# Kernel tuning notes

Measured on AMD Instinct MI355X. Metric: run time of the kernel, lower is better.

Reference implementation:

```python
import jax, jax.numpy as jnp
import numpy as np
import math

D_KEY = 64
D_VALUE = 64
NUM_HEADS = 16
D_MODEL = D_VALUE * NUM_HEADS  # 1024


def setup_inputs() -> dict:
    key = jax.random.key(0)
    ks = jax.random.split(key, 5)
    B, N = 2, 2048
    s = 1.0 / math.sqrt(D_MODEL)
    return {
        "x": jax.random.normal(ks[0], (B, N, D_MODEL), dtype=jnp.float32),
        "Wq": jax.random.normal(ks[1], (D_MODEL, D_KEY * NUM_HEADS), dtype=jnp.float32) * s,
        "Wk": jax.random.normal(ks[2], (D_MODEL, D_KEY * NUM_HEADS), dtype=jnp.float32) * s,
        "Wv": jax.random.normal(ks[3], (D_MODEL, D_MODEL), dtype=jnp.float32) * s,
        "Wp": jax.random.normal(ks[4], (D_MODEL, D_MODEL), dtype=jnp.float32) * s,
    }


def reference(x, Wq, Wk, Wv, Wp):
    # x: [B, N, d_model]. Equivalent to the original block-diagonal concat trick:
    # off-diagonal blocks are -inf, so softmax over the key axis reduces to
    # independent per-head softmax attention.
    B, N, D = x.shape
    H, K, V = NUM_HEADS, D_KEY, D_VALUE
    scale = 1.0 / math.sqrt(K)
    q = (x @ Wq).reshape(B, N, H, K)
    k = (x @ Wk).reshape(B, N, H, K)
    v = (x @ Wv).reshape(B, N, H, V)
    scores = jnp.einsum("bnhk,bmhk->bhnm", q, k) * scale  # [B,H,N,N]
    attn = jax.nn.softmax(scores, axis=-1)
    out = jnp.einsum("bhnm,bmhv->bnhv", attn, v).reshape(B, N, D)
    return x + out @ Wp
```

## Files before the change

### kernel.cpp

```cpp
#include <hip/hip_runtime.h>

typedef float f32x4 __attribute__((ext_vector_type(4)));
typedef __bf16 bf16x8 __attribute__((ext_vector_type(8)));

#define DEV static __device__ __forceinline__

DEV ushort f2bf(float f) {
  unsigned u = __builtin_bit_cast(unsigned, f);
  u += 0x7FFFu + ((u >> 16) & 1u);
  return (ushort)(u >> 16);
}

DEV bf16x8 ld_frag(const ushort* p) {
  return __builtin_bit_cast(bf16x8, *reinterpret_cast<const int4*>(p));
}

DEV bf16x8 ld_lds(const ushort* base, int byte_off) {
  return __builtin_bit_cast(bf16x8,
      *reinterpret_cast<const int4*>(reinterpret_cast<const char*>(base) + byte_off));
}

DEV int swz(int row, int col_byte) { return row * 128 + (col_byte ^ ((row & 7) << 4)); }

DEV float fast_exp2(float x) {
  float r;
  asm("v_exp_f32 %0, %1" : "=v"(r) : "v"(x));
  return r;
}

DEV unsigned cvt_pk_bf16(float lo, float hi) {
  unsigned r;
  asm("v_cvt_pk_bf16_f32 %0, %1, %2" : "=v"(r) : "v"(lo), "v"(hi));
  return r;
}

DEV void gload16(const ushort* g, ushort* l) {
  __builtin_amdgcn_global_load_lds(
      (const __attribute__((address_space(1))) unsigned int*)g,
      (__attribute__((address_space(3))) unsigned int*)l, 16, 0, 0);
}


__global__ __launch_bounds__(256) void prep(const float* __restrict__ x,
                                            const float* __restrict__ w0,
                                            const float* __restrict__ w1,
                                            const float* __restrict__ w2,
                                            const float* __restrict__ w3,
                                            ushort* __restrict__ xb,
                                            ushort* __restrict__ wt) {
  __shared__ float tile[32][33];
  const int z = blockIdx.z;
  const int tx = threadIdx.x, ty = threadIdx.y;
  if (z < 4) {
    const float* w = z == 0 ? w0 : z == 1 ? w1 : z == 2 ? w2 : w3;
    ushort* out = wt + (size_t)z * 1024 * 1024;
    const int n0 = blockIdx.x * 32, k0 = blockIdx.y * 32;
    float4 v = *reinterpret_cast<const float4*>(&w[(size_t)(k0 + ty) * 1024 + n0 + tx * 4]);
    tile[ty][tx * 4 + 0] = v.x;
    tile[ty][tx * 4 + 1] = v.y;
    tile[ty][tx * 4 + 2] = v.z;
    tile[ty][tx * 4 + 3] = v.w;
    __syncthreads();
    ushort4 o = make_ushort4(f2bf(tile[tx * 4 + 0][ty]), f2bf(tile[tx * 4 + 1][ty]),
                             f2bf(tile[tx * 4 + 2][ty]), f2bf(tile[tx * 4 + 3][ty]));
    *reinterpret_cast<ushort4*>(&out[(size_t)(n0 + ty) * 1024 + k0 + tx * 4]) = o;
  } else {
    const int blk = ((z - 4) * 32 + blockIdx.y) * 32 + blockIdx.x;
    const int tid = ty * 8 + tx;
    const int i = blk * 256 + tid;
    float4 v = reinterpret_cast<const float4*>(x)[i];
    ushort4 o = make_ushort4(f2bf(v.x), f2bf(v.y), f2bf(v.z), f2bf(v.w));
    reinterpret_cast<ushort4*>(xb)[i] = o;
  }
}


DEV void gemm_core64(const ushort* __restrict__ A, const ushort* __restrict__ BT,
                     ushort* a_lds, ushort* b_lds, int row0, int col0, f32x4 acc[4][2]) {
  const int tid = threadIdx.x;
  const int lane = tid & 63;
  const int w = tid >> 6, wr = w >> 1, wc = w & 1;
  const int lg = lane >> 4, l15 = lane & 15;
  const int sr8 = lane >> 3;
  const int scol = ((lane & 7) ^ sr8) << 3;
  const ushort* ga = A + (size_t)(row0 + w * 32 + sr8) * 1024 + scol;
  const ushort* gb = BT + (size_t)(col0 + w * 16 + sr8) * 1024 + scol;
#pragma unroll
  for (int ai = 0; ai < 4; ++ai)
#pragma unroll
    for (int bj = 0; bj < 2; ++bj) acc[ai][bj] = f32x4{0.f, 0.f, 0.f, 0.f};

  for (int kt = 0; kt < 1024; kt += 64) {
    __syncthreads();
#pragma unroll
    for (int p = 0; p < 4; ++p)
      gload16(ga + kt + (size_t)(p * 8) * 1024, a_lds + (w * 32 + p * 8) * 64);
#pragma unroll
    for (int p = 0; p < 2; ++p)
      gload16(gb + kt + (size_t)(p * 8) * 1024, b_lds + (w * 16 + p * 8) * 64);
    __syncthreads();
    bf16x8 af[4][2], bfr[2][2];
#pragma unroll
    for (int kk = 0; kk < 2; ++kk) {
#pragma unroll
      for (int i = 0; i < 4; ++i)
        af[i][kk] = ld_lds(a_lds, swz(wr * 64 + i * 16 + l15, kk * 64 + lg * 16));
#pragma unroll
      for (int j = 0; j < 2; ++j)
        bfr[j][kk] = ld_lds(b_lds, swz(wc * 32 + j * 16 + l15, kk * 64 + lg * 16));
    }
#pragma unroll
    for (int kk = 0; kk < 2; ++kk)
#pragma unroll
      for (int ai = 0; ai < 4; ++ai)
#pragma unroll
        for (int bj = 0; bj < 2; ++bj)
          acc[ai][bj] = __builtin_amdgcn_mfma_f32_16x16x32_bf16(af[ai][kk], bfr[bj][kk],
                                                                acc[ai][bj], 0, 0, 0);
  }
}

__global__ __launch_bounds__(256) void gemm_qkv(const ushort* __restrict__ xb,
                                                const ushort* __restrict__ wqT,
                                                const ushort* __restrict__ wkT,
                                                const ushort* __restrict__ wvT,
                                                ushort* __restrict__ q, ushort* __restrict__ k,
                                                ushort* __restrict__ vt) {
  __shared__ ushort a_lds[128 * 64], b_lds[64 * 64];
  const int fid = blockIdx.x;
  const int wid = (fid & 7) * 192 + (fid >> 3);
  const int row = wid / 48, rem = wid % 48;
  const int z = rem % 3, col = rem / 3;
  const int row0 = row * 128, col0 = col * 64;
  const ushort* BT = z == 0 ? wqT : z == 1 ? wkT : wvT;
  f32x4 acc[4][2];
  gemm_core64(xb, BT, a_lds, b_lds, row0, col0, acc);
  const int lane = threadIdx.x & 63;
  const int w = threadIdx.x >> 6, wr = w >> 1, wc = w & 1;
  const int lg = lane >> 4, l15 = lane & 15;
  if (z < 2) {
    ushort* out = z == 0 ? q : k;
    const float sc = z == 0 ? 0.125f * 1.4426950408889634f : 1.0f;
#pragma unroll
    for (int ai = 0; ai < 4; ++ai)
#pragma unroll
      for (int bj = 0; bj < 2; ++bj)
#pragma unroll
        for (int r = 0; r < 4; ++r) {
          int orow = row0 + wr * 64 + ai * 16 + lg * 4 + r;
          int ocol = col0 + wc * 32 + bj * 16 + l15;
          out[(size_t)orow * 1024 + ocol] = f2bf(acc[ai][bj][r] * sc);
        }
  } else {
#pragma unroll
    for (int ai = 0; ai < 4; ++ai)
#pragma unroll
      for (int bj = 0; bj < 2; ++bj) {
        int orow = row0 + wr * 64 + ai * 16 + lg * 4;
        int ocol = col0 + wc * 32 + bj * 16 + l15;
        int bb = orow >> 11, n = orow & 2047;
        ushort4 pk = make_ushort4(f2bf(acc[ai][bj][0]), f2bf(acc[ai][bj][1]),
                                  f2bf(acc[ai][bj][2]), f2bf(acc[ai][bj][3]));
        *reinterpret_cast<ushort4*>(vt + ((size_t)(bb * 1024 + ocol)) * 2048 + n) = pk;
      }
  }
}

__global__ __launch_bounds__(256) void gemm_out(const ushort* __restrict__ ob,
                                                const ushort* __restrict__ wpT,
                                                const float* __restrict__ x,
                                                float* __restrict__ y) {
  __shared__ ushort a_lds[64 * 64], b_lds[64 * 64];
  const int fid = blockIdx.x;
  const int wid = (fid & 7) * 128 + (fid >> 3);
  const int row0 = (wid >> 4) * 64, col0 = (wid & 15) * 64;
  const int tid = threadIdx.x;
  const int lane = tid & 63;
  const int w = tid >> 6, wr = w >> 1, wc = w & 1;
  const int lg = lane >> 4, l15 = lane & 15;
  const int sr8 = lane >> 3;
  const int scol = ((lane & 7) ^ sr8) << 3;
  const ushort* ga = ob + (size_t)(row0 + w * 16 + sr8) * 1024 + scol;
  const ushort* gb = wpT + (size_t)(col0 + w * 16 + sr8) * 1024 + scol;

  f32x4 acc[2][2];
#pragma unroll
  for (int ai = 0; ai < 2; ++ai)
#pragma unroll
    for (int bj = 0; bj < 2; ++bj) acc[ai][bj] = f32x4{0.f, 0.f, 0.f, 0.f};

  for (int kt = 0; kt < 1024; kt += 64) {
    __syncthreads();
#pragma unroll
    for (int p = 0; p < 2; ++p) {
      gload16(ga + kt + (size_t)(p * 8) * 1024, a_lds + (w * 16 + p * 8) * 64);
      gload16(gb + kt + (size_t)(p * 8) * 1024, b_lds + (w * 16 + p * 8) * 64);
    }
    __syncthreads();
    bf16x8 af[2][2], bfr[2][2];
#pragma unroll
    for (int kk = 0; kk < 2; ++kk) {
#pragma unroll
      for (int i = 0; i < 2; ++i) {
        af[i][kk] = ld_lds(a_lds, swz(wr * 32 + i * 16 + l15, kk * 64 + lg * 16));
        bfr[i][kk] = ld_lds(b_lds, swz(wc * 32 + i * 16 + l15, kk * 64 + lg * 16));
      }
    }
#pragma unroll
    for (int kk = 0; kk < 2; ++kk)
#pragma unroll
      for (int ai = 0; ai < 2; ++ai)
#pragma unroll
        for (int bj = 0; bj < 2; ++bj)
          acc[ai][bj] = __builtin_amdgcn_mfma_f32_16x16x32_bf16(af[ai][kk], bfr[bj][kk],
                                                                acc[ai][bj], 0, 0, 0);
  }

#pragma unroll
  for (int ai = 0; ai < 2; ++ai)
#pragma unroll
    for (int bj = 0; bj < 2; ++bj)
#pragma unroll
      for (int r = 0; r < 4; ++r) {
        int orow = row0 + wr * 32 + ai * 16 + lg * 4 + r;
        int ocol = col0 + wc * 32 + bj * 16 + l15;
        size_t idx = (size_t)orow * 1024 + ocol;
        y[idx] = x[idx] + acc[ai][bj][r];
      }
}

__global__ __launch_bounds__(256) void attn(const ushort* __restrict__ qg,
                                            const ushort* __restrict__ kg,
                                            const ushort* __restrict__ vtg,
                                            ushort* __restrict__ og) {
  __shared__ ushort k_lds[4 * 64 * 64];
  __shared__ ushort v_lds[4 * 64 * 64];
  const int fid = blockIdx.x;
  const int wid = (fid & 7) * 64 + (fid >> 3);
  const int bh = wid >> 4, q0 = wid & 15;
  const int b = bh >> 4, h = bh & 15;
  const int n0 = q0 * 128;
  const int tid = threadIdx.x, lane = tid & 63, w = tid >> 6;
  const int lg = lane >> 4, l15 = lane & 15;

  bf16x8 qf[2][2];
#pragma unroll
  for (int qi = 0; qi < 2; ++qi)
#pragma unroll
    for (int d32 = 0; d32 < 2; ++d32)
      qf[qi][d32] = ld_frag(qg + (size_t)(b * 2048 + n0 + w * 32 + qi * 16 + l15) * 1024 +
                            h * 64 + d32 * 32 + lg * 8);

  f32x4 o[2][4];
#pragma unroll
  for (int qi = 0; qi < 2; ++qi)
#pragma unroll
    for (int bj = 0; bj < 4; ++bj) o[qi][bj] = f32x4{0.f, 0.f, 0.f, 0.f};
  f32x4 ssum[2] = {f32x4{0.f, 0.f, 0.f, 0.f}, f32x4{0.f, 0.f, 0.f, 0.f}};

  const int sr8 = lane >> 3;
  const int scol = ((lane & 7) ^ sr8) << 3;
  const ushort* kbase = kg + (size_t)(b * 2048 + w * 16 + sr8) * 1024 + h * 64 + scol;
  const ushort* vbase = vtg + (size_t)(b * 1024 + h * 64 + w * 16 + sr8) * 2048 + scol;

  auto stage_sub = [&](ushort* kdst, ushort* vdst, int kv0) {
#pragma unroll
    for (int p = 0; p < 2; ++p) {
      gload16(kbase + (size_t)(kv0 + p * 8) * 1024, kdst + (w * 16 + p * 8) * 64);
      gload16(vbase + (size_t)(p * 8) * 2048 + kv0, vdst + (w * 16 + p * 8) * 64);
    }
  };
  auto stage2 = [&](int buf, int kv0) {
    stage_sub(k_lds + (2 * buf) * 4096, v_lds + (2 * buf) * 4096, kv0);
    stage_sub(k_lds + (2 * buf + 1) * 4096, v_lds + (2 * buf + 1) * 4096, kv0 + 64);
  };

  const int4 ones4 = make_int4(0x3F803F80, 0x3F803F80, 0x3F803F80, 0x3F803F80);
  const bf16x8 onesf = __builtin_bit_cast(bf16x8, ones4);

  auto qk_sub = [&](const ushort* kb, f32x4 s[2][4]) {
#pragma unroll
    for (int qi = 0; qi < 2; ++qi)
#pragma unroll
      for (int kj = 0; kj < 4; ++kj) s[qi][kj] = f32x4{0.f, 0.f, 0.f, 0.f};
#pragma unroll
    for (int d32 = 0; d32 < 2; ++d32)
#pragma unroll
      for (int kj = 0; kj < 4; ++kj) {
        bf16x8 kf = ld_lds(kb, swz(kj * 16 + l15, d32 * 64 + lg * 16));
        s[0][kj] = __builtin_amdgcn_mfma_f32_16x16x32_bf16(kf, qf[0][d32], s[0][kj], 0, 0, 0);
        s[1][kj] = __builtin_amdgcn_mfma_f32_16x16x32_bf16(kf, qf[1][d32], s[1][kj], 0, 0, 0);
      }
  };

  auto exp_pack = [&](f32x4 s[2][4], bf16x8 pa[2][2]) {
#pragma unroll
    for (int qi = 0; qi < 2; ++qi) {
      unsigned pk[4][2];
#pragma unroll
      for (int kj = 0; kj < 4; ++kj) {
        float p0 = fast_exp2(s[qi][kj][0]);
        float p1 = fast_exp2(s[qi][kj][1]);
        float p2 = fast_exp2(s[qi][kj][2]);
        float p3 = fast_exp2(s[qi][kj][3]);
        pk[kj][0] = cvt_pk_bf16(p0, p1);
        pk[kj][1] = cvt_pk_bf16(p2, p3);
      }
#pragma unroll
      for (int k32 = 0; k32 < 2; ++k32) {
        unsigned x0 = pk[2 * k32][0], y0 = pk[2 * k32 + 1][0];
        unsigned x1 = pk[2 * k32][1], y1 = pk[2 * k32 + 1][1];
        asm("v_permlane32_swap_b32 %0, %1" : "+v"(x0), "+v"(y0));
        asm("v_permlane32_swap_b32 %0, %1" : "+v"(x1), "+v"(y1));
        asm("v_permlane16_swap_b32 %0, %1" : "+v"(x0), "+v"(y0));
        asm("v_permlane16_swap_b32 %0, %1" : "+v"(x1), "+v"(y1));
        int4 fr = make_int4(x0, x1, y0, y1);
        pa[qi][k32] = __builtin_bit_cast(bf16x8, fr);
      }
    }
  };

  auto pv_only = [&](const ushort* vb, bf16x8 pa[2][2]) {
#pragma unroll
    for (int qi = 0; qi < 2; ++qi) {
      ssum[qi] = __builtin_amdgcn_mfma_f32_16x16x32_bf16(pa[qi][0], onesf, ssum[qi], 0, 0, 0);
      ssum[qi] = __builtin_amdgcn_mfma_f32_16x16x32_bf16(pa[qi][1], onesf, ssum[qi], 0, 0, 0);
    }
#pragma unroll
    for (int k32 = 0; k32 < 2; ++k32)
#pragma unroll
      for (int bj = 0; bj < 4; ++bj) {
        bf16x8 vf = ld_lds(vb, swz(bj * 16 + l15, k32 * 64 + lg * 16));
        o[0][bj] = __builtin_amdgcn_mfma_f32_16x16x32_bf16(pa[0][k32], vf, o[0][bj], 0, 0, 0);
        o[1][bj] = __builtin_amdgcn_mfma_f32_16x16x32_bf16(pa[1][k32], vf, o[1][bj], 0, 0, 0);
      }
  };

  auto body2 = [&](int buf) {
    const ushort* kb0 = k_lds + (2 * buf) * 4096;
    const ushort* kb1 = k_lds + (2 * buf + 1) * 4096;
    const ushort* vb0 = v_lds + (2 * buf) * 4096;
    const ushort* vb1 = v_lds + (2 * buf + 1) * 4096;
    f32x4 s0[2][4], s1[2][4];
    bf16x8 pa0[2][2], pa1[2][2];
    qk_sub(kb0, s0);
    qk_sub(kb1, s1);
    exp_pack(s0, pa0);
    pv_only(vb0, pa0);
    exp_pack(s1, pa1);
    pv_only(vb1, pa1);
    __builtin_amdgcn_sched_group_barrier(0x020, 8, 0);
    __builtin_amdgcn_sched_group_barrier(0x100, 8, 0);
    __builtin_amdgcn_sched_group_barrier(0x008, 16, 0);
    __builtin_amdgcn_sched_group_barrier(0x100, 8, 0);
#pragma unroll
    for (int i = 0; i < 16; ++i) {
      __builtin_amdgcn_sched_group_barrier(0x008, 1, 0);
      __builtin_amdgcn_sched_group_barrier(0x002, 4, 0);
    }
    __builtin_amdgcn_sched_group_barrier(0x100, 8, 0);
#pragma unroll
    for (int i = 0; i < 20; ++i) {
      __builtin_amdgcn_sched_group_barrier(0x008, 1, 0);
      __builtin_amdgcn_sched_group_barrier(0x002, 3, 0);
    }
    __builtin_amdgcn_sched_group_barrier(0x100, 8, 0);
    __builtin_amdgcn_sched_group_barrier(0x008, 20, 0);
  };

  stage2(0, 0);
  __syncthreads();

  for (int tt = 0; tt < 8; ++tt) {
    stage2(1, (2 * tt + 1) * 128);
    body2(0);
    __syncthreads();
    if (tt < 7) stage2(0, (2 * tt + 2) * 128);
    body2(1);
    __syncthreads();
  }

#pragma unroll
  for (int qi = 0; qi < 2; ++qi) {
    f32x4 inv;
#pragma unroll
    for (int r = 0; r < 4; ++r) inv[r] = 1.0f / ssum[qi][r];
#pragma unroll
    for (int bj = 0; bj < 4; ++bj)
#pragma unroll
      for (int r = 0; r < 4; ++r) {
        int n = n0 + w * 32 + qi * 16 + lg * 4 + r;
        og[(size_t)(b * 2048 + n) * 1024 + h * 64 + bj * 16 + l15] = f2bf(o[qi][bj][r] * inv[r]);
      }
  }
}


extern "C" void kernel_launch(void* const* d_in, const int* in_sizes, int n_in,
                              void* d_out, int out_size, void* d_ws, size_t ws_size,
                              hipStream_t stream) {
  const float* x = (const float*)d_in[0];
  const float* Wq = (const float*)d_in[1];
  const float* Wk = (const float*)d_in[2];
  const float* Wv = (const float*)d_in[3];
  const float* Wp = (const float*)d_in[4];
  float* y = (float*)d_out;

  char* ws = (char*)d_ws;
  ushort* xb = (ushort*)(ws);
  ushort* wT = (ushort*)(ws + (8ull << 20));
  ushort* qw = (ushort*)(ws + (16ull << 20));
  ushort* kw = (ushort*)(ws + (24ull << 20));
  ushort* vtw = (ushort*)(ws + (32ull << 20));
  ushort* ow = (ushort*)(ws);

  prep<<<dim3(32, 32, 8), dim3(8, 32), 0, stream>>>(x, Wq, Wk, Wv, Wp, xb, wT);
  gemm_qkv<<<1536, 256, 0, stream>>>(xb, wT, wT + (1u << 20), wT + (2u << 20), qw, kw, vtw);
  attn<<<512, 256, 0, stream>>>(qw, kw, vtw, ow);
  gemm_out<<<1024, 256, 0, stream>>>(ow, wT + (3u << 20), x, y);
}
```

Measured before the change: 105.6 us.

## Fuse Q/K/V projections into one block sharing the x tile

Each QKV GEMM block now computes the Q, K and V output tiles for the same row/column range in one pass, loading the x (A) tile into LDS once and reusing it across all three weight matrices. The grid shrinks from 1536 to 512 blocks and the block swizzle is adjusted. This removes two-thirds of the redundant A-tile loads, but triples the accumulator registers and increases LDS use, which may lower occupancy and leave fewer blocks to spread across the CUs.

```diff
diff --git a/kernel.cpp b/kernel.cpp
--- a/kernel.cpp
+++ b/kernel.cpp
@@ -74,21 +74,34 @@
   }
 }
 
-
-DEV void gemm_core64(const ushort* __restrict__ A, const ushort* __restrict__ BT,
-                     ushort* a_lds, ushort* b_lds, int row0, int col0, f32x4 acc[4][2]) {
+__global__ __launch_bounds__(256) void gemm_qkv(const ushort* __restrict__ xb,
+                                                const ushort* __restrict__ wT,
+                                                ushort* __restrict__ q, ushort* __restrict__ k,
+                                                ushort* __restrict__ vt) {
+  __shared__ ushort a_lds[128 * 64];
+  __shared__ ushort b_lds[3][64 * 64];
+  const int fid = blockIdx.x;
+  const int wid = (fid & 7) * 64 + (fid >> 3);
+  const int row0 = (wid >> 4) * 128, col0 = (wid & 15) * 64;
   const int tid = threadIdx.x;
   const int lane = tid & 63;
   const int w = tid >> 6, wr = w >> 1, wc = w & 1;
   const int lg = lane >> 4, l15 = lane & 15;
   const int sr8 = lane >> 3;
   const int scol = ((lane & 7) ^ sr8) << 3;
-  const ushort* ga = A + (size_t)(row0 + w * 32 + sr8) * 1024 + scol;
-  const ushort* gb = BT + (size_t)(col0 + w * 16 + sr8) * 1024 + scol;
-#pragma unroll
-  for (int ai = 0; ai < 4; ++ai)
-#pragma unroll
-    for (int bj = 0; bj < 2; ++bj) acc[ai][bj] = f32x4{0.f, 0.f, 0.f, 0.f};
+  const ushort* ga = xb + (size_t)(row0 + w * 32 + sr8) * 1024 + scol;
+  const ushort* gb[3];
+#pragma unroll
+  for (int z = 0; z < 3; ++z)
+    gb[z] = wT + (size_t)z * 1024 * 1024 + (size_t)(col0 + w * 16 + sr8) * 1024 + scol;
+
+  f32x4 acc[3][4][2];
+#pragma unroll
+  for (int z = 0; z < 3; ++z)
+#pragma unroll
+    for (int ai = 0; ai < 4; ++ai)
+#pragma unroll
+      for (int bj = 0; bj < 2; ++bj) acc[z][ai][bj] = f32x4{0.f, 0.f, 0.f, 0.f};
 
   for (int kt = 0; kt < 1024; kt += 64) {
     __syncthreads();
@@ -96,49 +109,38 @@
     for (int p = 0; p < 4; ++p)
       gload16(ga + kt + (size_t)(p * 8) * 1024, a_lds + (w * 32 + p * 8) * 64);
 #pragma unroll
-    for (int p = 0; p < 2; ++p)
-      gload16(gb + kt + (size_t)(p * 8) * 1024, b_lds + (w * 16 + p * 8) * 64);
-    __syncthreads();
-    bf16x8 af[4][2], bfr[2][2];
-#pragma unroll
-    for (int kk = 0; kk < 2; ++kk) {
+    for (int z = 0; z < 3; ++z)
+#pragma unroll
+      for (int p = 0; p < 2; ++p)
+        gload16(gb[z] + kt + (size_t)(p * 8) * 1024, b_lds[z] + (w * 16 + p * 8) * 64);
+    __syncthreads();
+    bf16x8 af[4][2];
+#pragma unroll
+    for (int kk = 0; kk < 2; ++kk)
 #pragma unroll
       for (int i = 0; i < 4; ++i)
         af[i][kk] = ld_lds(a_lds, swz(wr * 64 + i * 16 + l15, kk * 64 + lg * 16));
 #pragma unroll
-      for (int j = 0; j < 2; ++j)
-        bfr[j][kk] = ld_lds(b_lds, swz(wc * 32 + j * 16 + l15, kk * 64 + lg * 16));
-    }
-#pragma unroll
-    for (int kk = 0; kk < 2; ++kk)
-#pragma unroll
-      for (int ai = 0; ai < 4; ++ai)
-#pragma unroll
-        for (int bj = 0; bj < 2; ++bj)
-          acc[ai][bj] = __builtin_amdgcn_mfma_f32_16x16x32_bf16(af[ai][kk], bfr[bj][kk],
-                                                                acc[ai][bj], 0, 0, 0);
-  }
-}
-
-__global__ __launch_bounds__(256) void gemm_qkv(const ushort* __restrict__ xb,
-                                                const ushort* __restrict__ wqT,
-                                                const ushort* __restrict__ wkT,
-                                                const ushort* __restrict__ wvT,
-                                                ushort* __restrict__ q, ushort* __restrict__ k,
-                                                ushort* __restrict__ vt) {
-  __shared__ ushort a_lds[128 * 64], b_lds[64 * 64];
-  const int fid = blockIdx.x;
-  const int wid = (fid & 7) * 192 + (fid >> 3);
-  const int row = wid / 48, rem = wid % 48;
-  const int z = rem % 3, col = rem / 3;
-  const int row0 = row * 128, col0 = col * 64;
-  const ushort* BT = z == 0 ? wqT : z == 1 ? wkT : wvT;
-  f32x4 acc[4][2];
-  gemm_core64(xb, BT, a_lds, b_lds, row0, col0, acc);
-  const int lane = threadIdx.x & 63;
-  const int w = threadIdx.x >> 6, wr = w >> 1, wc = w & 1;
-  const int lg = lane >> 4, l15 = lane & 15;
-  if (z < 2) {
+    for (int z = 0; z < 3; ++z) {
+      bf16x8 bfr[2][2];
+#pragma unroll
+      for (int kk = 0; kk < 2; ++kk)
+#pragma unroll
+        for (int j = 0; j < 2; ++j)
+          bfr[j][kk] = ld_lds(b_lds[z], swz(wc * 32 + j * 16 + l15, kk * 64 + lg * 16));
+#pragma unroll
+      for (int kk = 0; kk < 2; ++kk)
+#pragma unroll
+        for (int ai = 0; ai < 4; ++ai)
+#pragma unroll
+          for (int bj = 0; bj < 2; ++bj)
+            acc[z][ai][bj] = __builtin_amdgcn_mfma_f32_16x16x32_bf16(af[ai][kk], bfr[bj][kk],
+                                                                     acc[z][ai][bj], 0, 0, 0);
+    }
+  }
+
+#pragma unroll
+  for (int z = 0; z < 2; ++z) {
     ushort* out = z == 0 ? q : k;
     const float sc = z == 0 ? 0.125f * 1.4426950408889634f : 1.0f;
 #pragma unroll
@@ -149,21 +151,20 @@
         for (int r = 0; r < 4; ++r) {
           int orow = row0 + wr * 64 + ai * 16 + lg * 4 + r;
           int ocol = col0 + wc * 32 + bj * 16 + l15;
-          out[(size_t)orow * 1024 + ocol] = f2bf(acc[ai][bj][r] * sc);
+          out[(size_t)orow * 1024 + ocol] = f2bf(acc[z][ai][bj][r] * sc);
         }
-  } else {
-#pragma unroll
-    for (int ai = 0; ai < 4; ++ai)
-#pragma unroll
-      for (int bj = 0; bj < 2; ++bj) {
-        int orow = row0 + wr * 64 + ai * 16 + lg * 4;
-        int ocol = col0 + wc * 32 + bj * 16 + l15;
-        int bb = orow >> 11, n = orow & 2047;
-        ushort4 pk = make_ushort4(f2bf(acc[ai][bj][0]), f2bf(acc[ai][bj][1]),
-                                  f2bf(acc[ai][bj][2]), f2bf(acc[ai][bj][3]));
-        *reinterpret_cast<ushort4*>(vt + ((size_t)(bb * 1024 + ocol)) * 2048 + n) = pk;
-      }
-  }
+  }
+#pragma unroll
+  for (int ai = 0; ai < 4; ++ai)
+#pragma unroll
+    for (int bj = 0; bj < 2; ++bj) {
+      int orow = row0 + wr * 64 + ai * 16 + lg * 4;
+      int ocol = col0 + wc * 32 + bj * 16 + l15;
+      int bb = orow >> 11, n = orow & 2047;
+      ushort4 pk = make_ushort4(f2bf(acc[2][ai][bj][0]), f2bf(acc[2][ai][bj][1]),
+                                f2bf(acc[2][ai][bj][2]), f2bf(acc[2][ai][bj][3]));
+      *reinterpret_cast<ushort4*>(vt + ((size_t)(bb * 1024 + ocol)) * 2048 + n) = pk;
+    }
 }
 
 __global__ __launch_bounds__(256) void gemm_out(const ushort* __restrict__ ob,
@@ -415,7 +416,7 @@
   ushort* ow = (ushort*)(ws);
 
   prep<<<dim3(32, 32, 8), dim3(8, 32), 0, stream>>>(x, Wq, Wk, Wv, Wp, xb, wT);
-  gemm_qkv<<<1536, 256, 0, stream>>>(xb, wT, wT + (1u << 20), wT + (2u << 20), qw, kw, vtw);
+  gemm_qkv<<<512, 256, 0, stream>>>(xb, wT, qw, kw, vtw);
   attn<<<512, 256, 0, stream>>>(qw, kw, vtw, ow);
   gemm_out<<<1024, 256, 0, stream>>>(ow, wT + (3u << 20), x, y);
 }
```

Measured after the change: 102.8 us. -2.7%, faster.
